# Kernel optimization log

Hardware: AMD Instinct MI355X
Metric: run time of the kernel (lower is better)

Reference implementation:

```python
import jax, jax.numpy as jnp
import numpy as np

B, N, C, H, W = 16, 64, 128, 64, 64
IMG = 512.0
SCALE = 0.125          # spatial_scale
MAX_GRID = 16          # >= ceil(max_roi_side * SCALE); boxes built so sides <= 128px -> 16
OUT_CH = 256


def setup_inputs() -> dict:
    key = jax.random.key(0)
    k1, k2, k3, k4, k5 = jax.random.split(key, 5)
    z = jax.random.normal(k1, (B, C, H, W), jnp.float32)
    xy = jax.random.uniform(k2, (B, N, 2), jnp.float32, 0.0, IMG - 128.0)
    wh = jax.random.uniform(k3, (B, N, 2), jnp.float32, 8.0, 128.0)
    bboxes = jnp.concatenate([xy, xy + wh], axis=-1)  # [B,N,4] xyxy, image coords
    W_out = jax.random.normal(k4, (OUT_CH, C), jnp.float32) / np.sqrt(C).astype(np.float32)
    b_out = jax.random.normal(k5, (OUT_CH,), jnp.float32) * 0.01
    return {"z": z, "bboxes": bboxes, "W_out": W_out, "b_out": b_out}


def _prep_coord(c, L):
    # torchvision bilinear edge handling; c: sample coord, L: spatial extent
    inr = (c > -1.0) & (c < float(L))          # out of range -> value 0 (still counted)
    cc = jnp.clip(c, 0.0, None)
    lo = jnp.minimum(jnp.floor(cc).astype(jnp.int32), L - 1)
    hi = jnp.minimum(lo + 1, L - 1)
    cc = jnp.where(lo >= L - 1, lo.astype(c.dtype), cc)
    frac = cc - lo.astype(c.dtype)
    return lo, hi, frac, inr


def roi_align_1x1(z, boxes, scale=SCALE, max_grid=MAX_GRID):
    # z: [B,C,H,W], boxes: [B,N,4] xyxy. torchvision roi_align, output_size=1,
    # aligned=True, sampling_ratio=-1 (adaptive grid = ceil(roi_side), masked to max_grid).
    Bz, Cz, Hh, Ww = z.shape
    b = boxes * scale - 0.5                       # aligned=True offset
    x1, y1, x2, y2 = b[..., 0], b[..., 1], b[..., 2], b[..., 3]
    roi_w, roi_h = x2 - x1, y2 - y1               # [B,N]
    gw = jnp.clip(jnp.ceil(roi_w), 1.0, float(max_grid))
    gh = jnp.clip(jnp.ceil(roi_h), 1.0, float(max_grid))
    g = jnp.arange(max_grid, dtype=z.dtype)
    sy = y1[..., None] + (g + 0.5) * (roi_h / gh)[..., None]   # [B,N,G]
    sx = x1[..., None] + (g + 0.5) * (roi_w / gw)[..., None]
    vy = g < gh[..., None]                        # grid-validity (adaptive count)
    vx = g < gw[..., None]

    yl, yh, fy, iry = _prep_coord(sy, Hh)
    xl, xh, fx, irx = _prep_coord(sx, Ww)
    hy, hx = 1.0 - fy, 1.0 - fx

    zf = z.transpose(0, 2, 3, 1)                  # [B,H,W,C]
    shp = (Bz, boxes.shape[1], max_grid, max_grid)
    Yl = jnp.broadcast_to(yl[..., :, None], shp)
    Yh = jnp.broadcast_to(yh[..., :, None], shp)
    Xl = jnp.broadcast_to(xl[..., None, :], shp)
    Xh = jnp.broadcast_to(xh[..., None, :], shp)

    gather = jax.vmap(lambda zb, yi, xi: zb[yi, xi])   # -> [B,N,G,G,C]
    v11 = gather(zf, Yl, Xl)
    v12 = gather(zf, Yl, Xh)
    v21 = gather(zf, Yh, Xl)
    v22 = gather(zf, Yh, Xh)

    w11 = hy[..., :, None] * hx[..., None, :]
    w12 = hy[..., :, None] * fx[..., None, :]
    w21 = fy[..., :, None] * hx[..., None, :]
    w22 = fy[..., :, None] * fx[..., None, :]
    val = (w11[..., None] * v11 + w12[..., None] * v12
           + w21[..., None] * v21 + w22[..., None] * v22)   # [B,N,G,G,C]

    mask = ((vy[..., :, None] & vx[..., None, :])
            & (iry[..., :, None] & irx[..., None, :])).astype(z.dtype)
    val = val * mask[..., None]
    count = (gh * gw)[..., None]                   # adaptive sample count
    return val.sum(axis=(2, 3)) / count            # [B,N,C]


def reference(z, bboxes, W_out, b_out):
    # roi_align (output 1x1) -> avgpool(1) is identity -> reshape [B,N,C] -> Linear
    feats = roi_align_1x1(z, bboxes)               # [B,N,C]
    return feats @ W_out.T + b_out                 # [B,N,OUT_CH]
```

## Files before the change

kernel.cpp:

```cpp
#include <hip/hip_runtime.h>

#define B_ 16
#define N_ 64
#define C_ 128
#define H_ 64
#define W_ 64
#define HW_ (H_ * W_)
#define OUT_CH_ 256
#define MAX_GRID_ 16
#define SCALE_ 0.125f

__device__ __forceinline__ unsigned short f2bf(float f) {
  unsigned int u = __float_as_uint(f);
  u = (u + 0x7fffu + ((u >> 16) & 1u)) >> 16;
  return (unsigned short)u;
}

__global__ __launch_bounds__(256) void transpose_bf16_kernel(
    const float* __restrict__ z, unsigned short* __restrict__ zf) {
  __shared__ unsigned short tile[128 * 129];
  const int b  = blockIdx.y;
  const int pt = blockIdx.x;
  const int t  = threadIdx.x;

  const float* zb = z + (size_t)b * C_ * HW_;
#pragma unroll
  for (int iter = 0; iter < 16; ++iter) {
    int idx = iter * 256 + t;
    int c   = idx >> 5;
    int p4  = (idx & 31) << 2;
    float4 v = *(const float4*)(zb + (size_t)c * HW_ + pt * 128 + p4);
    tile[(p4 + 0) * 129 + c] = f2bf(v.x);
    tile[(p4 + 1) * 129 + c] = f2bf(v.y);
    tile[(p4 + 2) * 129 + c] = f2bf(v.z);
    tile[(p4 + 3) * 129 + c] = f2bf(v.w);
  }
  __syncthreads();

  unsigned short* zfb = zf + (size_t)b * HW_ * C_;
#pragma unroll
  for (int iter = 0; iter < 8; ++iter) {
    int idx = iter * 256 + t;
    int p   = idx >> 4;
    int k8  = (idx & 15) << 3;
    const unsigned short* src = &tile[p * 129 + k8];
    uint4 u;
    u.x = (unsigned int)src[0] | ((unsigned int)src[1] << 16);
    u.y = (unsigned int)src[2] | ((unsigned int)src[3] << 16);
    u.z = (unsigned int)src[4] | ((unsigned int)src[5] << 16);
    u.w = (unsigned int)src[6] | ((unsigned int)src[7] << 16);
    *(uint4*)(zfb + (size_t)(pt * 128 + p) * C_ + k8) = u;
  }
}

__global__ __launch_bounds__(256) void wtrans_kernel(
    const float* __restrict__ Wm, float* __restrict__ Wt) {
  __shared__ float tile[32][33];
  int ot = blockIdx.x;
  int ct = blockIdx.y;
  int j = threadIdx.x, i0 = threadIdx.y;
#pragma unroll
  for (int k = 0; k < 4; ++k) {
    int i = i0 + k * 8;
    tile[i][j] = Wm[(size_t)(ot * 32 + i) * C_ + ct * 32 + j];
  }
  __syncthreads();
#pragma unroll
  for (int k = 0; k < 4; ++k) {
    int i = i0 + k * 8;
    Wt[(size_t)(ct * 32 + i) * OUT_CH_ + ot * 32 + j] = tile[j][i];
  }
}

__global__ __launch_bounds__(256) void roi_fused_kernel(
    const unsigned short* __restrict__ zf,
    const float* __restrict__ boxes,
    const float* __restrict__ Wt,
    const float* __restrict__ bias,
    float* __restrict__ out)
{
  int roi = blockIdx.x;
  int t   = threadIdx.x;
  int wv  = t >> 6;
  int c2  = t & 63;
  int co  = c2 << 1;

  float4 bx = ((const float4*)boxes)[roi];
  float x1 = bx.x * SCALE_ - 0.5f;
  float y1 = bx.y * SCALE_ - 0.5f;
  float roi_w = bx.z * SCALE_ - 0.5f - x1;
  float roi_h = bx.w * SCALE_ - 0.5f - y1;
  float gwf = fminf(fmaxf(ceilf(roi_w), 1.0f), (float)MAX_GRID_);
  float ghf = fminf(fmaxf(ceilf(roi_h), 1.0f), (float)MAX_GRID_);
  int gw = (int)gwf;
  int gh = (int)ghf;
  float stepx = roi_w / gwf;
  float stepy = roi_h / ghf;

  const unsigned short* zb = zf + (size_t)(roi >> 6) * (HW_ * C_);

  float acc0 = 0.0f, acc1 = 0.0f;
  for (int gy = wv; gy < gh; gy += 4) {
    float sy = y1 + ((float)gy + 0.5f) * stepy;
    float wy = (sy > -1.0f && sy < (float)H_) ? 1.0f : 0.0f;
    float cy = fmaxf(sy, 0.0f);
    int yl = (int)cy;
    yl = yl < (H_ - 1) ? yl : (H_ - 1);
    int yh = (yl + 1) < (H_ - 1) ? (yl + 1) : (H_ - 1);
    if (yl >= H_ - 1) cy = (float)yl;
    float fy = cy - (float)yl;
    float hy = 1.0f - fy;
    const unsigned short* rowl = zb + (size_t)yl * W_ * C_;
    const unsigned short* rowh = zb + (size_t)yh * W_ * C_;

    for (int gx = 0; gx < gw; ++gx) {
      float sx = x1 + ((float)gx + 0.5f) * stepx;
      float wx = (sx > -1.0f && sx < (float)W_) ? 1.0f : 0.0f;
      float cx = fmaxf(sx, 0.0f);
      int xl = (int)cx;
      xl = xl < (W_ - 1) ? xl : (W_ - 1);
      int xh = (xl + 1) < (W_ - 1) ? (xl + 1) : (W_ - 1);
      if (xl >= W_ - 1) cx = (float)xl;
      float fx = cx - (float)xl;
      float hx = 1.0f - fx;

      float m   = wy * wx;
      float w11 = hy * hx * m, w12 = hy * fx * m;
      float w21 = fy * hx * m, w22 = fy * fx * m;
      unsigned int v11 = *(const unsigned int*)(rowl + xl * C_ + co);
      unsigned int v12 = *(const unsigned int*)(rowl + xh * C_ + co);
      unsigned int v21 = *(const unsigned int*)(rowh + xl * C_ + co);
      unsigned int v22 = *(const unsigned int*)(rowh + xh * C_ + co);

      acc0 += w11 * __uint_as_float(v11 << 16)
            + w12 * __uint_as_float(v12 << 16)
            + w21 * __uint_as_float(v21 << 16)
            + w22 * __uint_as_float(v22 << 16);
      acc1 += w11 * __uint_as_float(v11 & 0xffff0000u)
            + w12 * __uint_as_float(v12 & 0xffff0000u)
            + w21 * __uint_as_float(v21 & 0xffff0000u)
            + w22 * __uint_as_float(v22 & 0xffff0000u);
    }
  }

  __shared__ float red[4][128];
  __shared__ float feat[128];
  red[wv][co]     = acc0;
  red[wv][co + 1] = acc1;
  __syncthreads();
  if (t < 128) {
    feat[t] = (red[0][t] + red[1][t] + red[2][t] + red[3][t])
              * (1.0f / (ghf * gwf));
  }
  __syncthreads();

  float s0 = bias[t], s1 = 0.0f, s2 = 0.0f, s3 = 0.0f;
#pragma unroll 4
  for (int k = 0; k < C_; k += 4) {
    s0 += feat[k + 0] * Wt[(size_t)(k + 0) * OUT_CH_ + t];
    s1 += feat[k + 1] * Wt[(size_t)(k + 1) * OUT_CH_ + t];
    s2 += feat[k + 2] * Wt[(size_t)(k + 2) * OUT_CH_ + t];
    s3 += feat[k + 3] * Wt[(size_t)(k + 3) * OUT_CH_ + t];
  }
  out[(size_t)roi * OUT_CH_ + t] = (s0 + s1) + (s2 + s3);
}

extern "C" void kernel_launch(void* const* d_in, const int* in_sizes, int n_in,
                              void* d_out, int out_size, void* d_ws, size_t ws_size,
                              hipStream_t stream) {
  const float* z     = (const float*)d_in[0];
  const float* boxes = (const float*)d_in[1];
  const float* Wm    = (const float*)d_in[2];
  const float* bias  = (const float*)d_in[3];
  float* out = (float*)d_out;

  char* ws = (char*)d_ws;
  unsigned short* zf = (unsigned short*)ws;
  float* Wt = (float*)(ws + (size_t)B_ * HW_ * C_ * 2);

  transpose_bf16_kernel<<<dim3(HW_ / 128, B_), 256, 0, stream>>>(z, zf);
  wtrans_kernel<<<dim3(OUT_CH_ / 32, C_ / 32), dim3(32, 8), 0, stream>>>(Wm, Wt);
  roi_fused_kernel<<<B_ * N_, 256, 0, stream>>>(zf, boxes, Wt, bias, out);
}
```

Baseline: 112.1 us.

## Split ROI gather across grid rows and batch the linear layer per block

The gather now runs one 128-thread block per pair of sampling rows of each ROI, about 8k blocks, instead of one block per ROI walking every row serially. Block IDs are remapped so each image's blocks land on the same XCD, and blocks past the ROI's grid height exit early. Per-row partial sums go to a workspace buffer. A new final kernel reduces those partials and runs the linear layer for four ROIs per block, so each Wt load is reused four times. The weight transpose is folded into the feature transpose launch to save one launch. The cost is an extra global round trip for the partials and one more kernel boundary.

After: 109.4 us. -2.4%, faster.

```diff
diff --git a/kernel.cpp b/kernel.cpp
--- a/kernel.cpp
+++ b/kernel.cpp
@@ -16,13 +16,33 @@
   return (unsigned short)u;
 }
 
-__global__ __launch_bounds__(256) void transpose_bf16_kernel(
-    const float* __restrict__ z, unsigned short* __restrict__ zf) {
+__global__ __launch_bounds__(256) void transpose_kernel(
+    const float* __restrict__ z, const float* __restrict__ Wm,
+    unsigned short* __restrict__ zf, float* __restrict__ Wt) {
   __shared__ unsigned short tile[128 * 129];
+  const int t = threadIdx.x;
+
+  if (blockIdx.y == 16) {
+    float* ft = (float*)tile;
+    int x  = blockIdx.x;
+    int ot = x & 7, ct = x >> 3;
+    int j = t & 31, i0 = t >> 5;
+#pragma unroll
+    for (int k = 0; k < 4; ++k) {
+      int i = i0 + k * 8;
+      ft[i * 33 + j] = Wm[(size_t)(ot * 32 + i) * C_ + ct * 32 + j];
+    }
+    __syncthreads();
+#pragma unroll
+    for (int k = 0; k < 4; ++k) {
+      int i = i0 + k * 8;
+      Wt[(size_t)(ct * 32 + i) * OUT_CH_ + ot * 32 + j] = ft[j * 33 + i];
+    }
+    return;
+  }
+
   const int b  = blockIdx.y;
   const int pt = blockIdx.x;
-  const int t  = threadIdx.x;
-
   const float* zb = z + (size_t)b * C_ * HW_;
 #pragma unroll
   for (int iter = 0; iter < 16; ++iter) {
@@ -53,37 +73,21 @@
   }
 }
 
-__global__ __launch_bounds__(256) void wtrans_kernel(
-    const float* __restrict__ Wm, float* __restrict__ Wt) {
-  __shared__ float tile[32][33];
-  int ot = blockIdx.x;
-  int ct = blockIdx.y;
-  int j = threadIdx.x, i0 = threadIdx.y;
-#pragma unroll
-  for (int k = 0; k < 4; ++k) {
-    int i = i0 + k * 8;
-    tile[i][j] = Wm[(size_t)(ot * 32 + i) * C_ + ct * 32 + j];
-  }
-  __syncthreads();
-#pragma unroll
-  for (int k = 0; k < 4; ++k) {
-    int i = i0 + k * 8;
-    Wt[(size_t)(ct * 32 + i) * OUT_CH_ + ot * 32 + j] = tile[j][i];
-  }
-}
-
-__global__ __launch_bounds__(256) void roi_fused_kernel(
+__global__ __launch_bounds__(128) void gather_kernel(
     const unsigned short* __restrict__ zf,
     const float* __restrict__ boxes,
-    const float* __restrict__ Wt,
-    const float* __restrict__ bias,
-    float* __restrict__ out)
+    float* __restrict__ partial)
 {
-  int roi = blockIdx.x;
-  int t   = threadIdx.x;
-  int wv  = t >> 6;
-  int c2  = t & 63;
-  int co  = c2 << 1;
+  int bid  = blockIdx.x;
+  int xcd  = bid & 7;
+  int slot = bid >> 3;
+  int img  = xcd + ((slot >> 9) << 3);
+  int s    = slot & 511;
+  int roi  = img * N_ + (s >> 3);
+  int t    = threadIdx.x;
+  int gy   = ((s & 7) << 1) + (t >> 6);
+  int c2   = t & 63;
+  int co   = c2 << 1;
 
   float4 bx = ((const float4*)boxes)[roi];
   float x1 = bx.x * SCALE_ - 0.5f;
@@ -94,75 +98,101 @@
   float ghf = fminf(fmaxf(ceilf(roi_h), 1.0f), (float)MAX_GRID_);
   int gw = (int)gwf;
   int gh = (int)ghf;
+  if (gy >= gh) return;
+
   float stepx = roi_w / gwf;
   float stepy = roi_h / ghf;
 
+  float sy = y1 + ((float)gy + 0.5f) * stepy;
+  float wy = (sy > -1.0f && sy < (float)H_) ? 1.0f : 0.0f;
+  float cy = fmaxf(sy, 0.0f);
+  int yl = (int)cy;
+  yl = yl < (H_ - 1) ? yl : (H_ - 1);
+  int yh = (yl + 1) < (H_ - 1) ? (yl + 1) : (H_ - 1);
+  if (yl >= H_ - 1) cy = (float)yl;
+  float fy = cy - (float)yl;
+  float hy = 1.0f - fy;
+
   const unsigned short* zb = zf + (size_t)(roi >> 6) * (HW_ * C_);
+  const unsigned short* rowl = zb + (size_t)yl * W_ * C_;
+  const unsigned short* rowh = zb + (size_t)yh * W_ * C_;
 
   float acc0 = 0.0f, acc1 = 0.0f;
-  for (int gy = wv; gy < gh; gy += 4) {
-    float sy = y1 + ((float)gy + 0.5f) * stepy;
-    float wy = (sy > -1.0f && sy < (float)H_) ? 1.0f : 0.0f;
-    float cy = fmaxf(sy, 0.0f);
-    int yl = (int)cy;
-    yl = yl < (H_ - 1) ? yl : (H_ - 1);
-    int yh = (yl + 1) < (H_ - 1) ? (yl + 1) : (H_ - 1);
-    if (yl >= H_ - 1) cy = (float)yl;
-    float fy = cy - (float)yl;
-    float hy = 1.0f - fy;
-    const unsigned short* rowl = zb + (size_t)yl * W_ * C_;
-    const unsigned short* rowh = zb + (size_t)yh * W_ * C_;
-
-    for (int gx = 0; gx < gw; ++gx) {
-      float sx = x1 + ((float)gx + 0.5f) * stepx;
-      float wx = (sx > -1.0f && sx < (float)W_) ? 1.0f : 0.0f;
-      float cx = fmaxf(sx, 0.0f);
-      int xl = (int)cx;
-      xl = xl < (W_ - 1) ? xl : (W_ - 1);
-      int xh = (xl + 1) < (W_ - 1) ? (xl + 1) : (W_ - 1);
-      if (xl >= W_ - 1) cx = (float)xl;
-      float fx = cx - (float)xl;
-      float hx = 1.0f - fx;
-
-      float m   = wy * wx;
-      float w11 = hy * hx * m, w12 = hy * fx * m;
-      float w21 = fy * hx * m, w22 = fy * fx * m;
-      unsigned int v11 = *(const unsigned int*)(rowl + xl * C_ + co);
-      unsigned int v12 = *(const unsigned int*)(rowl + xh * C_ + co);
-      unsigned int v21 = *(const unsigned int*)(rowh + xl * C_ + co);
-      unsigned int v22 = *(const unsigned int*)(rowh + xh * C_ + co);
-
-      acc0 += w11 * __uint_as_float(v11 << 16)
-            + w12 * __uint_as_float(v12 << 16)
-            + w21 * __uint_as_float(v21 << 16)
-            + w22 * __uint_as_float(v22 << 16);
-      acc1 += w11 * __uint_as_float(v11 & 0xffff0000u)
-            + w12 * __uint_as_float(v12 & 0xffff0000u)
-            + w21 * __uint_as_float(v21 & 0xffff0000u)
-            + w22 * __uint_as_float(v22 & 0xffff0000u);
-    }
-  }
-
-  __shared__ float red[4][128];
-  __shared__ float feat[128];
-  red[wv][co]     = acc0;
-  red[wv][co + 1] = acc1;
+  for (int gx = 0; gx < gw; ++gx) {
+    float sx = x1 + ((float)gx + 0.5f) * stepx;
+    float wx = (sx > -1.0f && sx < (float)W_) ? 1.0f : 0.0f;
+    float cx = fmaxf(sx, 0.0f);
+    int xl = (int)cx;
+    xl = xl < (W_ - 1) ? xl : (W_ - 1);
+    int xh = (xl + 1) < (W_ - 1) ? (xl + 1) : (W_ - 1);
+    if (xl >= W_ - 1) cx = (float)xl;
+    float fx = cx - (float)xl;
+    float hx = 1.0f - fx;
+
+    float m   = wy * wx;
+    float w11 = hy * hx * m, w12 = hy * fx * m;
+    float w21 = fy * hx * m, w22 = fy * fx * m;
+    unsigned int v11 = *(const unsigned int*)(rowl + xl * C_ + co);
+    unsigned int v12 = *(const unsigned int*)(rowl + xh * C_ + co);
+    unsigned int v21 = *(const unsigned int*)(rowh + xl * C_ + co);
+    unsigned int v22 = *(const unsigned int*)(rowh + xh * C_ + co);
+
+    acc0 += w11 * __uint_as_float(v11 << 16)
+          + w12 * __uint_as_float(v12 << 16)
+          + w21 * __uint_as_float(v21 << 16)
+          + w22 * __uint_as_float(v22 << 16);
+    acc1 += w11 * __uint_as_float(v11 & 0xffff0000u)
+          + w12 * __uint_as_float(v12 & 0xffff0000u)
+          + w21 * __uint_as_float(v21 & 0xffff0000u)
+          + w22 * __uint_as_float(v22 & 0xffff0000u);
+  }
+
+  *(float2*)(partial + (size_t)(roi * MAX_GRID_ + gy) * C_ + co)
+      = make_float2(acc0, acc1);
+}
+
+__global__ __launch_bounds__(256) void final_kernel(
+    const float* __restrict__ partial,
+    const float* __restrict__ boxes,
+    const float* __restrict__ Wt,
+    const float* __restrict__ bias,
+    float* __restrict__ out)
+{
+  int rbase = blockIdx.x << 2;
+  int t  = threadIdx.x;
+  int c  = t & 127;
+  int r2 = t >> 7;
+
+  __shared__ float feat[4][128];
+#pragma unroll
+  for (int rr = 0; rr < 2; ++rr) {
+    int r   = r2 * 2 + rr;
+    int roi = rbase + r;
+    float4 bx = ((const float4*)boxes)[roi];
+    float gwf = fminf(fmaxf(ceilf((bx.z - bx.x) * SCALE_), 1.0f), (float)MAX_GRID_);
+    float ghf = fminf(fmaxf(ceilf((bx.w - bx.y) * SCALE_), 1.0f), (float)MAX_GRID_);
+    int gh = (int)ghf;
+    float s = 0.0f;
+    for (int gy = 0; gy < gh; ++gy)
+      s += partial[(size_t)(roi * MAX_GRID_ + gy) * C_ + c];
+    feat[r][c] = s * (1.0f / (ghf * gwf));
+  }
   __syncthreads();
-  if (t < 128) {
-    feat[t] = (red[0][t] + red[1][t] + red[2][t] + red[3][t])
-              * (1.0f / (ghf * gwf));
-  }
-  __syncthreads();
-
-  float s0 = bias[t], s1 = 0.0f, s2 = 0.0f, s3 = 0.0f;
+
+  float bv = bias[t];
+  float a0 = 0.0f, a1 = 0.0f, a2 = 0.0f, a3 = 0.0f;
 #pragma unroll 4
-  for (int k = 0; k < C_; k += 4) {
-    s0 += feat[k + 0] * Wt[(size_t)(k + 0) * OUT_CH_ + t];
-    s1 += feat[k + 1] * Wt[(size_t)(k + 1) * OUT_CH_ + t];
-    s2 += feat[k + 2] * Wt[(size_t)(k + 2) * OUT_CH_ + t];
-    s3 += feat[k + 3] * Wt[(size_t)(k + 3) * OUT_CH_ + t];
-  }
-  out[(size_t)roi * OUT_CH_ + t] = (s0 + s1) + (s2 + s3);
+  for (int k = 0; k < C_; ++k) {
+    float w = Wt[(size_t)k * OUT_CH_ + t];
+    a0 += feat[0][k] * w;
+    a1 += feat[1][k] * w;
+    a2 += feat[2][k] * w;
+    a3 += feat[3][k] * w;
+  }
+  out[(size_t)(rbase + 0) * OUT_CH_ + t] = a0 + bv;
+  out[(size_t)(rbase + 1) * OUT_CH_ + t] = a1 + bv;
+  out[(size_t)(rbase + 2) * OUT_CH_ + t] = a2 + bv;
+  out[(size_t)(rbase + 3) * OUT_CH_ + t] = a3 + bv;
 }
 
 extern "C" void kernel_launch(void* const* d_in, const int* in_sizes, int n_in,
@@ -176,9 +206,11 @@
 
   char* ws = (char*)d_ws;
   unsigned short* zf = (unsigned short*)ws;
-  float* Wt = (float*)(ws + (size_t)B_ * HW_ * C_ * 2);
-
-  transpose_bf16_kernel<<<dim3(HW_ / 128, B_), 256, 0, stream>>>(z, zf);
-  wtrans_kernel<<<dim3(OUT_CH_ / 32, C_ / 32), dim3(32, 8), 0, stream>>>(Wm, Wt);
-  roi_fused_kernel<<<B_ * N_, 256, 0, stream>>>(zf, boxes, Wt, bias, out);
-}
+  float* partial = (float*)(ws + (size_t)B_ * HW_ * C_ * 2);
+  float* Wt = (float*)(ws + (size_t)B_ * HW_ * C_ * 2
+                          + (size_t)B_ * N_ * MAX_GRID_ * C_ * 4);
+
+  transpose_kernel<<<dim3(HW_ / 128, B_ + 1), 256, 0, stream>>>(z, Wm, zf, Wt);
+  gather_kernel<<<B_ * N_ * (MAX_GRID_ / 2), 128, 0, stream>>>(zf, boxes, partial);
+  final_kernel<<<B_ * N_ / 4, 256, 0, stream>>>(partial, boxes, Wt, bias, out);
+}
```

## Merge weight transpose into feature transpose, widen ROI blocks, remap ROI order

Applied to the files above, without the earlier changes.

The weight-transpose kernel becomes an extra row of blocks in the feature-transpose launch, which removes one kernel launch. The ROI kernel now uses 512 threads, so 8 waves split the grid rows and two halves split the linear-layer reduction. Block indices are remapped so that consecutive blocks take ROIs from 8 different images, which changes L2 locality across the gathered feature map. The price is more shared memory and an extra sync, plus some imbalance for small ROIs where many waves sit idle.

New measurement: 99.37 us. -11.4%, faster.

```diff
diff --git a/kernel.cpp b/kernel.cpp
--- a/kernel.cpp
+++ b/kernel.cpp
@@ -16,13 +16,33 @@
   return (unsigned short)u;
 }
 
-__global__ __launch_bounds__(256) void transpose_bf16_kernel(
-    const float* __restrict__ z, unsigned short* __restrict__ zf) {
+__global__ __launch_bounds__(256) void transpose_kernel(
+    const float* __restrict__ z, const float* __restrict__ Wm,
+    unsigned short* __restrict__ zf, float* __restrict__ Wt) {
   __shared__ unsigned short tile[128 * 129];
+  const int t = threadIdx.x;
+
+  if (blockIdx.y == 16) {
+    float* ft = (float*)tile;
+    int x  = blockIdx.x;
+    int ot = x & 7, ct = x >> 3;
+    int j = t & 31, i0 = t >> 5;
+#pragma unroll
+    for (int k = 0; k < 4; ++k) {
+      int i = i0 + k * 8;
+      ft[i * 33 + j] = Wm[(size_t)(ot * 32 + i) * C_ + ct * 32 + j];
+    }
+    __syncthreads();
+#pragma unroll
+    for (int k = 0; k < 4; ++k) {
+      int i = i0 + k * 8;
+      Wt[(size_t)(ct * 32 + i) * OUT_CH_ + ot * 32 + j] = ft[j * 33 + i];
+    }
+    return;
+  }
+
   const int b  = blockIdx.y;
   const int pt = blockIdx.x;
-  const int t  = threadIdx.x;
-
   const float* zb = z + (size_t)b * C_ * HW_;
 #pragma unroll
   for (int iter = 0; iter < 16; ++iter) {
@@ -53,37 +73,19 @@
   }
 }
 
-__global__ __launch_bounds__(256) void wtrans_kernel(
-    const float* __restrict__ Wm, float* __restrict__ Wt) {
-  __shared__ float tile[32][33];
-  int ot = blockIdx.x;
-  int ct = blockIdx.y;
-  int j = threadIdx.x, i0 = threadIdx.y;
-#pragma unroll
-  for (int k = 0; k < 4; ++k) {
-    int i = i0 + k * 8;
-    tile[i][j] = Wm[(size_t)(ot * 32 + i) * C_ + ct * 32 + j];
-  }
-  __syncthreads();
-#pragma unroll
-  for (int k = 0; k < 4; ++k) {
-    int i = i0 + k * 8;
-    Wt[(size_t)(ct * 32 + i) * OUT_CH_ + ot * 32 + j] = tile[j][i];
-  }
-}
-
-__global__ __launch_bounds__(256) void roi_fused_kernel(
+__global__ __launch_bounds__(512) void roi_fused_kernel(
     const unsigned short* __restrict__ zf,
     const float* __restrict__ boxes,
     const float* __restrict__ Wt,
     const float* __restrict__ bias,
     float* __restrict__ out)
 {
-  int roi = blockIdx.x;
+  int bid = blockIdx.x;
+  int img = (bid & 7) | ((bid >> 9) << 3);
+  int roi = img * N_ + ((bid >> 3) & 63);
   int t   = threadIdx.x;
   int wv  = t >> 6;
-  int c2  = t & 63;
-  int co  = c2 << 1;
+  int co  = (t & 63) << 1;
 
   float4 bx = ((const float4*)boxes)[roi];
   float x1 = bx.x * SCALE_ - 0.5f;
@@ -97,10 +99,10 @@
   float stepx = roi_w / gwf;
   float stepy = roi_h / ghf;
 
-  const unsigned short* zb = zf + (size_t)(roi >> 6) * (HW_ * C_);
+  const unsigned short* zb = zf + (size_t)img * (HW_ * C_);
 
   float acc0 = 0.0f, acc1 = 0.0f;
-  for (int gy = wv; gy < gh; gy += 4) {
+  for (int gy = wv; gy < gh; gy += 8) {
     float sy = y1 + ((float)gy + 0.5f) * stepy;
     float wy = (sy > -1.0f && sy < (float)H_) ? 1.0f : 0.0f;
     float cy = fmaxf(sy, 0.0f);
@@ -110,8 +112,8 @@
     if (yl >= H_ - 1) cy = (float)yl;
     float fy = cy - (float)yl;
     float hy = 1.0f - fy;
-    const unsigned short* rowl = zb + (size_t)yl * W_ * C_;
-    const unsigned short* rowh = zb + (size_t)yh * W_ * C_;
+    const unsigned short* rowl = zb + (size_t)yl * W_ * C_ + co;
+    const unsigned short* rowh = zb + (size_t)yh * W_ * C_ + co;
 
     for (int gx = 0; gx < gw; ++gx) {
       float sx = x1 + ((float)gx + 0.5f) * stepx;
@@ -127,10 +129,10 @@
       float m   = wy * wx;
       float w11 = hy * hx * m, w12 = hy * fx * m;
       float w21 = fy * hx * m, w22 = fy * fx * m;
-      unsigned int v11 = *(const unsigned int*)(rowl + xl * C_ + co);
-      unsigned int v12 = *(const unsigned int*)(rowl + xh * C_ + co);
-      unsigned int v21 = *(const unsigned int*)(rowh + xl * C_ + co);
-      unsigned int v22 = *(const unsigned int*)(rowh + xh * C_ + co);
+      unsigned int v11 = *(const unsigned int*)(rowl + (xl << 7));
+      unsigned int v12 = *(const unsigned int*)(rowl + (xh << 7));
+      unsigned int v21 = *(const unsigned int*)(rowh + (xl << 7));
+      unsigned int v22 = *(const unsigned int*)(rowh + (xh << 7));
 
       acc0 += w11 * __uint_as_float(v11 << 16)
             + w12 * __uint_as_float(v12 << 16)
@@ -143,26 +145,31 @@
     }
   }
 
-  __shared__ float red[4][128];
+  __shared__ float red[8][128];
   __shared__ float feat[128];
+  __shared__ float lin[2][256];
   red[wv][co]     = acc0;
   red[wv][co + 1] = acc1;
   __syncthreads();
   if (t < 128) {
-    feat[t] = (red[0][t] + red[1][t] + red[2][t] + red[3][t])
-              * (1.0f / (ghf * gwf));
+    float s = (red[0][t] + red[1][t]) + (red[2][t] + red[3][t])
+            + (red[4][t] + red[5][t]) + (red[6][t] + red[7][t]);
+    feat[t] = s * (1.0f / (ghf * gwf));
   }
   __syncthreads();
 
-  float s0 = bias[t], s1 = 0.0f, s2 = 0.0f, s3 = 0.0f;
-#pragma unroll 4
-  for (int k = 0; k < C_; k += 4) {
-    s0 += feat[k + 0] * Wt[(size_t)(k + 0) * OUT_CH_ + t];
-    s1 += feat[k + 1] * Wt[(size_t)(k + 1) * OUT_CH_ + t];
-    s2 += feat[k + 2] * Wt[(size_t)(k + 2) * OUT_CH_ + t];
-    s3 += feat[k + 3] * Wt[(size_t)(k + 3) * OUT_CH_ + t];
-  }
-  out[(size_t)roi * OUT_CH_ + t] = (s0 + s1) + (s2 + s3);
+  int oc   = t & 255;
+  int half = t >> 8;
+  const float* wp = Wt + (size_t)(half * 64) * OUT_CH_ + oc;
+  const float* fp = feat + half * 64;
+  float a = 0.0f;
+#pragma unroll 8
+  for (int k = 0; k < 64; ++k)
+    a += fp[k] * wp[(size_t)k * OUT_CH_];
+  lin[half][oc] = a;
+  __syncthreads();
+  if (t < 256)
+    out[(size_t)roi * OUT_CH_ + t] = lin[0][t] + lin[1][t] + bias[t];
 }
 
 extern "C" void kernel_launch(void* const* d_in, const int* in_sizes, int n_in,
@@ -178,7 +185,6 @@
   unsigned short* zf = (unsigned short*)ws;
   float* Wt = (float*)(ws + (size_t)B_ * HW_ * C_ * 2);
 
-  transpose_bf16_kernel<<<dim3(HW_ / 128, B_), 256, 0, stream>>>(z, zf);
-  wtrans_kernel<<<dim3(OUT_CH_ / 32, C_ / 32), dim3(32, 8), 0, stream>>>(Wm, Wt);
-  roi_fused_kernel<<<B_ * N_, 256, 0, stream>>>(zf, boxes, Wt, bias, out);
+  transpose_kernel<<<dim3(HW_ / 128, B_ + 1), 256, 0, stream>>>(z, Wm, zf, Wt);
+  roi_fused_kernel<<<B_ * N_, 512, 0, stream>>>(zf, boxes, Wt, bias, out);
 }
```
